# Performance work log

Measured on AMD Instinct MI355X. Metric: run time of the kernel, lower is better.

Reference implementation:

```python
import jax, jax.numpy as jnp
import numpy as np

D_MODEL = 1024
NUM_HEADS = 16
DK = D_MODEL // NUM_HEADS
B, S = 2, 2048


def _init_w(key, out_f, in_f):
    std = 2.0 / (in_f + out_f) ** 0.5
    w = jax.random.truncated_normal(key, -3.0, 3.0, (out_f, in_f), dtype=jnp.float32)
    return w * std


def setup_inputs() -> dict:
    key = jax.random.key(0)
    kx, kq, kk, kv, ko = jax.random.split(key, 5)
    return {
        "x": jax.random.normal(kx, (B, S, D_MODEL), dtype=jnp.float32),
        "Wq": _init_w(kq, D_MODEL, D_MODEL),
        "Wk": _init_w(kk, D_MODEL, D_MODEL),
        "Wv": _init_w(kv, D_MODEL, D_MODEL),
        "Wo": _init_w(ko, D_MODEL, D_MODEL),
    }


def reference(x, Wq, Wk, Wv, Wo):
    b, s, _ = x.shape
    # Linear: einsum('... d_in, d_out d_in -> ... d_out')
    q = jnp.einsum("bsd,ed->bse", x, Wq)
    k = jnp.einsum("bsd,ed->bse", x, Wk)
    v = jnp.einsum("bsd,ed->bse", x, Wv)
    # split heads: [b, s, h*dk] -> [b, h, s, dk]
    q = q.reshape(b, s, NUM_HEADS, DK).transpose(0, 2, 1, 3)
    k = k.reshape(b, s, NUM_HEADS, DK).transpose(0, 2, 1, 3)
    v = v.reshape(b, s, NUM_HEADS, DK).transpose(0, 2, 1, 3)
    scores = jnp.einsum("bhqd,bhkd->bhqk", q, k) / (DK ** 0.5)
    causal = jnp.tril(jnp.ones((s, s), dtype=bool))
    scores = jnp.where(causal, scores, -jnp.inf)
    wei = jax.nn.softmax(scores, axis=-1)
    attn = jnp.einsum("bhqk,bhkd->bhqd", wei, v)
    attn = attn.transpose(0, 2, 1, 3).reshape(b, s, NUM_HEADS * DK)
    return jnp.einsum("bsd,ed->bse", attn, Wo)
```

## Files before the change

kernel.cpp:

```cpp
#include <hip/hip_runtime.h>
#include <hip/hip_bf16.h>
#include <math.h>

typedef __bf16 bf16;
typedef __attribute__((ext_vector_type(8))) __bf16 bf16x8;
typedef __attribute__((ext_vector_type(4))) __bf16 bf16x4;
typedef __attribute__((ext_vector_type(4))) float f32x4;

#define NHEAD 16
#define DKH 64
#define SEQ 2048
#define DMODEL 1024

__device__ __forceinline__ void gl_lds16(const void* g, void* lds) {
  __builtin_amdgcn_global_load_lds(
      (const __attribute__((address_space(1))) unsigned int*)g,
      (__attribute__((address_space(3))) unsigned int*)lds, 16, 0, 0);
}

__global__ void cvt5_kernel(const float* __restrict__ x, const float* __restrict__ wq,
                            const float* __restrict__ wk, const float* __restrict__ wv,
                            const float* __restrict__ wo, bf16* __restrict__ xb,
                            bf16* __restrict__ wqb, bf16* __restrict__ wkb,
                            bf16* __restrict__ wvb, bf16* __restrict__ wob) {
  int i = blockIdx.x * blockDim.x + threadIdx.x;
  const float* src; bf16* dst; int li;
  if (i < 1048576)      { src = x;  dst = xb;  li = i; }
  else if (i < 1310720) { src = wq; dst = wqb; li = i - 1048576; }
  else if (i < 1572864) { src = wk; dst = wkb; li = i - 1310720; }
  else if (i < 1835008) { src = wv; dst = wvb; li = i - 1572864; }
  else                  { src = wo; dst = wob; li = i - 1835008; }
  float4 v = ((const float4*)src)[li];
  bf16x4 o = { (bf16)v.x, (bf16)v.y, (bf16)v.z, (bf16)v.w };
  ((bf16x4*)dst)[li] = o;
}

__device__ __forceinline__ bf16x8 lds_frag(const bf16* T, int row, int gran) {
  return *(const bf16x8*)&T[row * 64 + ((gran ^ (row & 7)) << 3)];
}

template<int MODE>
__global__ __launch_bounds__(256) void gemm_nt(const bf16* __restrict__ A,
                                               const bf16* __restrict__ Bw,
                                               float* __restrict__ Cf,
                                               bf16* __restrict__ Cq,
                                               bf16* __restrict__ Ck,
                                               bf16* __restrict__ Cv,
                                               int M, int N, int K) {
  __shared__ __attribute__((aligned(16))) bf16 As[128 * 64];
  __shared__ __attribute__((aligned(16))) bf16 Bs[128 * 64];
  const int t = threadIdx.x;
  const int w = t >> 6, l = t & 63;
  const int wr = w >> 1, wc = w & 1;
  const int lin = blockIdx.y * gridDim.x + blockIdx.x;
  const int cpx = (gridDim.x * gridDim.y) >> 3;
  const int swz = (lin & 7) * cpx + (lin >> 3);
  const int tm = (swz / gridDim.x) * 128, tn = (swz % gridDim.x) * 128;
  const int c16 = l & 15, g4 = l >> 4, r8 = l >> 3;
  const int sg = ((l & 7) ^ (r8 & 7)) * 8;

  f32x4 acc[4][4];
#pragma unroll
  for (int i = 0; i < 4; ++i)
#pragma unroll
    for (int j = 0; j < 4; ++j) acc[i][j] = f32x4{0.f, 0.f, 0.f, 0.f};

  for (int k0 = 0; k0 < K; k0 += 64) {
#pragma unroll
    for (int c = 0; c < 4; ++c) {
      const int r0 = w * 32 + c * 8;
      gl_lds16(A + (size_t)(tm + r0 + r8) * K + k0 + sg, &As[r0 * 64]);
      gl_lds16(Bw + (size_t)(tn + r0 + r8) * K + k0 + sg, &Bs[r0 * 64]);
    }
    __syncthreads();
#pragma unroll
    for (int h = 0; h < 2; ++h) {
      bf16x8 af[4], bfr[4];
#pragma unroll
      for (int i = 0; i < 4; ++i)
        af[i] = lds_frag(As, wr * 64 + i * 16 + c16, h * 4 + g4);
#pragma unroll
      for (int j = 0; j < 4; ++j)
        bfr[j] = lds_frag(Bs, wc * 64 + j * 16 + c16, h * 4 + g4);
#pragma unroll
      for (int i = 0; i < 4; ++i)
#pragma unroll
        for (int j = 0; j < 4; ++j)
          acc[i][j] = __builtin_amdgcn_mfma_f32_16x16x32_bf16(af[i], bfr[j], acc[i][j], 0, 0, 0);
    }
    __syncthreads();
  }

  const int which = tn >> 10;
#pragma unroll
  for (int i = 0; i < 4; ++i) {
    const int row0 = tm + wr * 64 + i * 16 + g4 * 4;
#pragma unroll
    for (int j = 0; j < 4; ++j) {
      const int col = tn + wc * 64 + j * 16 + c16;
      if (MODE == 0) {
#pragma unroll
        for (int r = 0; r < 4; ++r) Cf[(size_t)(row0 + r) * N + col] = acc[i][j][r];
      } else {
        const int lc = col & 1023;
        if (which == 2) {
          const int bb = row0 >> 11, s = row0 & 2047;
          const int hh = lc >> 6, dk = lc & 63;
          bf16x4 o = { (bf16)acc[i][j][0], (bf16)acc[i][j][1],
                       (bf16)acc[i][j][2], (bf16)acc[i][j][3] };
          *(bf16x4*)&Cv[((size_t)(bb * NHEAD + hh) * DKH + dk) * SEQ + s] = o;
        } else {
          bf16* dst = which ? Ck : Cq;
#pragma unroll
          for (int r = 0; r < 4; ++r)
            dst[(size_t)(row0 + r) * DMODEL + lc] = (bf16)acc[i][j][r];
        }
      }
    }
  }
}

__device__ __forceinline__ f32x4 vmax4(f32x4 a, f32x4 b) {
  return f32x4{ fmaxf(a[0], b[0]), fmaxf(a[1], b[1]),
                fmaxf(a[2], b[2]), fmaxf(a[3], b[3]) };
}

__global__ __launch_bounds__(256) void attn_kernel(const bf16* __restrict__ qb,
                                                   const bf16* __restrict__ kb,
                                                   const bf16* __restrict__ vT,
                                                   bf16* __restrict__ ob) {
  __shared__ __attribute__((aligned(16))) bf16 Kt[2][64 * 64];
  __shared__ __attribute__((aligned(16))) bf16 Vt[2][64 * 64];
  __shared__ __attribute__((aligned(16))) bf16 Pb[4][16 * 64];
  const int w = threadIdx.x >> 6, l = threadIdx.x & 63;
  const int lin = blockIdx.x;
  const int swz = (lin & 7) * 64 + (lin >> 3);
  const int pr = swz & 15, h = (swz >> 4) & 15, b = swz >> 8;
  const int qtA = 31 - pr, qtB = pr;
  const int c16 = l & 15, g4 = l >> 4, r8 = l >> 3;
  const int sg = ((l & 7) ^ (r8 & 7)) * 8;

  const float SC2 = 0.125f * 1.44269504089f;
  const float THR = 8.0f / SC2;

  const bf16 oneb = (bf16)1.0f;
  const bf16x8 ones = { oneb, oneb, oneb, oneb, oneb, oneb, oneb, oneb };

  const bf16* kbase = kb + (size_t)b * SEQ * DMODEL + h * DKH;
  const bf16* vbase = vT + (size_t)(b * NHEAD + h) * DKH * SEQ;

  bf16x8 qfA[2], qfB[2];
#pragma unroll
  for (int d = 0; d < 2; ++d) {
    qfA[d] = *(const bf16x8*)(qb + (size_t)(b * SEQ + qtA * 64 + w * 16 + c16) * DMODEL +
                              h * DKH + d * 32 + g4 * 8);
    qfB[d] = *(const bf16x8*)(qb + (size_t)(b * SEQ + qtB * 64 + w * 16 + c16) * DMODEL +
                              h * DKH + d * 32 + g4 * 8);
  }

  auto stage = [&](int buf, int t) {
    const int kt0 = t * 64;
#pragma unroll
    for (int c = 0; c < 2; ++c) {
      const int row = w * 16 + c * 8;
      gl_lds16(kbase + (size_t)(kt0 + row + r8) * DMODEL + sg, &Kt[buf][row * 64]);
      gl_lds16(vbase + (size_t)(row + r8) * SEQ + kt0 + sg, &Vt[buf][row * 64]);
    }
  };

  stage(0, 0);
  __syncthreads();

  float mm = -INFINITY;
  f32x4 lsum4 = f32x4{0.f, 0.f, 0.f, 0.f};
  f32x4 acc[4];
#pragma unroll
  for (int n = 0; n < 4; ++n) acc[n] = f32x4{0.f, 0.f, 0.f, 0.f};

  const int TA = qtA + 1, TT = TA + qtB + 1;
  const int ql = w * 16 + c16;

  for (int tt = 0; tt < TT; ++tt) {
    const int cur = tt & 1;
    if (tt + 1 < TT) stage(cur ^ 1, (tt + 1 < TA) ? tt + 1 : tt + 1 - TA);
    const bool pA = tt < TA;
    const int t_in = pA ? tt : tt - TA;
    const bool diag = (t_in == (pA ? qtA : qtB));
    const bf16x8 q0 = pA ? qfA[0] : qfB[0];
    const bf16x8 q1 = pA ? qfA[1] : qfB[1];

    f32x4 s[4];
    __builtin_amdgcn_s_setprio(1);
#pragma unroll
    for (int j = 0; j < 4; ++j) {
      bf16x8 kf0 = lds_frag(Kt[cur], j * 16 + c16, g4);
      bf16x8 kf1 = lds_frag(Kt[cur], j * 16 + c16, 4 + g4);
      f32x4 c = f32x4{0.f, 0.f, 0.f, 0.f};
      c = __builtin_amdgcn_mfma_f32_16x16x32_bf16(kf0, q0, c, 0, 0, 0);
      c = __builtin_amdgcn_mfma_f32_16x16x32_bf16(kf1, q1, c, 0, 0, 0);
      s[j] = c;
    }
    __builtin_amdgcn_s_setprio(0);
    if (diag) {
#pragma unroll
      for (int j = 0; j < 4; ++j)
#pragma unroll
        for (int r = 0; r < 4; ++r)
          if (j * 16 + g4 * 4 + r > ql) s[j][r] = -INFINITY;
    }
    f32x4 t01 = vmax4(s[0], s[1]);
    f32x4 t23 = vmax4(s[2], s[3]);
    f32x4 tv = vmax4(t01, t23);
    float v = fmaxf(fmaxf(tv[0], tv[1]), fmaxf(tv[2], tv[3]));
    v = fmaxf(v, __shfl_xor(v, 16));
    v = fmaxf(v, __shfl_xor(v, 32));
    if (!__all(v <= mm + THR)) {
      const float mn = fmaxf(mm, v);
      const float scl = __builtin_amdgcn_exp2f(SC2 * (mm - mn));
      float sc4[4];
#pragma unroll
      for (int r = 0; r < 4; ++r) sc4[r] = __shfl(scl, g4 * 4 + r);
#pragma unroll
      for (int n = 0; n < 4; ++n)
#pragma unroll
        for (int r = 0; r < 4; ++r) acc[n][r] *= sc4[r];
#pragma unroll
      for (int r = 0; r < 4; ++r) lsum4[r] *= sc4[r];
      mm = mn;
    }
    const float nb = SC2 * mm;
    bf16* P = &Pb[w][0];
#pragma unroll
    for (int j = 0; j < 4; ++j) {
      bf16x4 pk;
#pragma unroll
      for (int r = 0; r < 4; ++r)
        pk[r] = (bf16)__builtin_amdgcn_exp2f(fmaf(s[j][r], SC2, -nb));
      const int col = j * 16 + g4 * 4;
      *(bf16x4*)&P[c16 * 64 + (((col >> 3) ^ (c16 & 7)) << 3) + (col & 7)] = pk;
    }
    bf16x8 pa0 = lds_frag(P, c16, g4);
    bf16x8 pa1 = lds_frag(P, c16, 4 + g4);
    __builtin_amdgcn_s_setprio(1);
#pragma unroll
    for (int n = 0; n < 4; ++n) {
      bf16x8 vf0 = lds_frag(Vt[cur], n * 16 + c16, g4);
      bf16x8 vf1 = lds_frag(Vt[cur], n * 16 + c16, 4 + g4);
      acc[n] = __builtin_amdgcn_mfma_f32_16x16x32_bf16(pa0, vf0, acc[n], 0, 0, 0);
      acc[n] = __builtin_amdgcn_mfma_f32_16x16x32_bf16(pa1, vf1, acc[n], 0, 0, 0);
    }
    lsum4 = __builtin_amdgcn_mfma_f32_16x16x32_bf16(pa0, ones, lsum4, 0, 0, 0);
    lsum4 = __builtin_amdgcn_mfma_f32_16x16x32_bf16(pa1, ones, lsum4, 0, 0, 0);
    __builtin_amdgcn_s_setprio(0);

    if (tt == TA - 1) {
#pragma unroll
      for (int n = 0; n < 4; ++n)
#pragma unroll
        for (int r = 0; r < 4; ++r) {
          float o = acc[n][r] / lsum4[r];
          ob[(size_t)(b * SEQ + qtA * 64 + w * 16 + g4 * 4 + r) * DMODEL +
             h * DKH + n * 16 + c16] = (bf16)o;
          acc[n][r] = 0.f;
        }
      lsum4 = f32x4{0.f, 0.f, 0.f, 0.f};
      mm = -INFINITY;
    }
    __syncthreads();
  }

#pragma unroll
  for (int n = 0; n < 4; ++n)
#pragma unroll
    for (int r = 0; r < 4; ++r) {
      float o = acc[n][r] / lsum4[r];
      ob[(size_t)(b * SEQ + qtB * 64 + w * 16 + g4 * 4 + r) * DMODEL +
         h * DKH + n * 16 + c16] = (bf16)o;
    }
}

extern "C" void kernel_launch(void* const* d_in, const int* in_sizes, int n_in,
                              void* d_out, int out_size, void* d_ws, size_t ws_size,
                              hipStream_t stream) {
  const float* x  = (const float*)d_in[0];
  const float* Wq = (const float*)d_in[1];
  const float* Wk = (const float*)d_in[2];
  const float* Wv = (const float*)d_in[3];
  const float* Wo = (const float*)d_in[4];
  float* out = (float*)d_out;
  char* ws = (char*)d_ws;
  const size_t MB = (size_t)1 << 20;

  bf16* xb   = (bf16*)(ws + 0 * MB);
  bf16* wqb  = (bf16*)(ws + 8 * MB);
  bf16* wkb  = (bf16*)(ws + 10 * MB);
  bf16* wvb  = (bf16*)(ws + 12 * MB);
  bf16* wob  = (bf16*)(ws + 14 * MB);
  bf16* qbuf = (bf16*)(ws + 16 * MB);
  bf16* kbuf = (bf16*)(ws + 24 * MB);
  bf16* vTb  = (bf16*)(ws + 32 * MB);
  bf16* abuf = (bf16*)(ws + 40 * MB);

  cvt5_kernel<<<8192, 256, 0, stream>>>(x, Wq, Wk, Wv, Wo, xb, wqb, wkb, wvb, wob);

  gemm_nt<3><<<dim3(3072 / 128, 4096 / 128), 256, 0, stream>>>(
      xb, wqb, nullptr, qbuf, kbuf, vTb, 4096, 3072, 1024);

  attn_kernel<<<dim3(512), 256, 0, stream>>>(qbuf, kbuf, vTb, abuf);

  gemm_nt<0><<<dim3(1024 / 128, 4096 / 128), 256, 0, stream>>>(
      abuf, wob, out, nullptr, nullptr, nullptr, 4096, 1024, 1024);
}
```

Before: 181.8 us.

## Split attention KV tiles across two wave groups and double-buffer GEMM LDS

The attention kernel moves to 512 threads. Two groups of four waves each handle alternating 64-key tiles inside a 128-key step, and at the end of each query tile their partial softmax states (max, sum, accumulator) are merged through LDS. This doubles the waves working on each query tile, to hide latency and cut the serial KV loop length. Separately, the QKV/output GEMM gains double-buffered LDS staging, so the next K-slice loads while the current one is being multiplied. The costs are extra LDS use and merge synchronisation, wasted work for the odd group on diagonal tiles, and the partner accumulator rounded to bf16 during the merge.

Measured after the change: 181.4 us. Within noise of the previous version (-0.2%).

```diff
diff --git a/kernel.cpp b/kernel.cpp
--- a/kernel.cpp
+++ b/kernel.cpp
@@ -47,8 +47,8 @@
                                                bf16* __restrict__ Ck,
                                                bf16* __restrict__ Cv,
                                                int M, int N, int K) {
-  __shared__ __attribute__((aligned(16))) bf16 As[128 * 64];
-  __shared__ __attribute__((aligned(16))) bf16 Bs[128 * 64];
+  __shared__ __attribute__((aligned(16))) bf16 As[2][128 * 64];
+  __shared__ __attribute__((aligned(16))) bf16 Bs[2][128 * 64];
   const int t = threadIdx.x;
   const int w = t >> 6, l = t & 63;
   const int wr = w >> 1, wc = w & 1;
@@ -65,23 +65,31 @@
 #pragma unroll
     for (int j = 0; j < 4; ++j) acc[i][j] = f32x4{0.f, 0.f, 0.f, 0.f};
 
-  for (int k0 = 0; k0 < K; k0 += 64) {
+  auto stage = [&](int buf, int k0) {
 #pragma unroll
     for (int c = 0; c < 4; ++c) {
       const int r0 = w * 32 + c * 8;
-      gl_lds16(A + (size_t)(tm + r0 + r8) * K + k0 + sg, &As[r0 * 64]);
-      gl_lds16(Bw + (size_t)(tn + r0 + r8) * K + k0 + sg, &Bs[r0 * 64]);
-    }
-    __syncthreads();
-#pragma unroll
-    for (int h = 0; h < 2; ++h) {
+      gl_lds16(A + (size_t)(tm + r0 + r8) * K + k0 + sg, &As[buf][r0 * 64]);
+      gl_lds16(Bw + (size_t)(tn + r0 + r8) * K + k0 + sg, &Bs[buf][r0 * 64]);
+    }
+  };
+
+  const int NK = K >> 6;
+  stage(0, 0);
+  __syncthreads();
+
+  for (int kt = 0; kt < NK; ++kt) {
+    const int cur = kt & 1;
+    if (kt + 1 < NK) stage(cur ^ 1, (kt + 1) << 6);
+#pragma unroll
+    for (int hh = 0; hh < 2; ++hh) {
       bf16x8 af[4], bfr[4];
 #pragma unroll
       for (int i = 0; i < 4; ++i)
-        af[i] = lds_frag(As, wr * 64 + i * 16 + c16, h * 4 + g4);
+        af[i] = lds_frag(As[cur], wr * 64 + i * 16 + c16, hh * 4 + g4);
 #pragma unroll
       for (int j = 0; j < 4; ++j)
-        bfr[j] = lds_frag(Bs, wc * 64 + j * 16 + c16, h * 4 + g4);
+        bfr[j] = lds_frag(Bs[cur], wc * 64 + j * 16 + c16, hh * 4 + g4);
 #pragma unroll
       for (int i = 0; i < 4; ++i)
 #pragma unroll
@@ -125,14 +133,17 @@
                 fmaxf(a[2], b[2]), fmaxf(a[3], b[3]) };
 }
 
-__global__ __launch_bounds__(256) void attn_kernel(const bf16* __restrict__ qb,
-                                                   const bf16* __restrict__ kb,
-                                                   const bf16* __restrict__ vT,
-                                                   bf16* __restrict__ ob) {
-  __shared__ __attribute__((aligned(16))) bf16 Kt[2][64 * 64];
-  __shared__ __attribute__((aligned(16))) bf16 Vt[2][64 * 64];
-  __shared__ __attribute__((aligned(16))) bf16 Pb[4][16 * 64];
+__global__ __launch_bounds__(512, 4) void attn_kernel(const bf16* __restrict__ qb,
+                                                      const bf16* __restrict__ kb,
+                                                      const bf16* __restrict__ vT,
+                                                      bf16* __restrict__ ob) {
+  __shared__ __attribute__((aligned(16))) bf16 Ke[2][64 * 64];
+  __shared__ __attribute__((aligned(16))) bf16 Ko[2][64 * 64];
+  __shared__ __attribute__((aligned(16))) bf16 Ve[2][64 * 64];
+  __shared__ __attribute__((aligned(16))) bf16 Vo[2][64 * 64];
+  __shared__ __attribute__((aligned(16))) bf16 Pb[8][16 * 64];
   const int w = threadIdx.x >> 6, l = threadIdx.x & 63;
+  const int g = w >> 2, wq = w & 3;
   const int lin = blockIdx.x;
   const int swz = (lin & 7) * 64 + (lin >> 3);
   const int pr = swz & 15, h = (swz >> 4) & 15, b = swz >> 8;
@@ -152,20 +163,19 @@
   bf16x8 qfA[2], qfB[2];
 #pragma unroll
   for (int d = 0; d < 2; ++d) {
-    qfA[d] = *(const bf16x8*)(qb + (size_t)(b * SEQ + qtA * 64 + w * 16 + c16) * DMODEL +
+    qfA[d] = *(const bf16x8*)(qb + (size_t)(b * SEQ + qtA * 64 + wq * 16 + c16) * DMODEL +
                               h * DKH + d * 32 + g4 * 8);
-    qfB[d] = *(const bf16x8*)(qb + (size_t)(b * SEQ + qtB * 64 + w * 16 + c16) * DMODEL +
+    qfB[d] = *(const bf16x8*)(qb + (size_t)(b * SEQ + qtB * 64 + wq * 16 + c16) * DMODEL +
                               h * DKH + d * 32 + g4 * 8);
   }
 
-  auto stage = [&](int buf, int t) {
-    const int kt0 = t * 64;
-#pragma unroll
-    for (int c = 0; c < 2; ++c) {
-      const int row = w * 16 + c * 8;
-      gl_lds16(kbase + (size_t)(kt0 + row + r8) * DMODEL + sg, &Kt[buf][row * 64]);
-      gl_lds16(vbase + (size_t)(row + r8) * SEQ + kt0 + sg, &Vt[buf][row * 64]);
-    }
+  auto stage = [&](int buf, int t128) {
+    const int kt0 = t128 * 128;
+    const int row = w * 8;
+    gl_lds16(kbase + (size_t)(kt0 + row + r8) * DMODEL + sg, &Ke[buf][row * 64]);
+    gl_lds16(kbase + (size_t)(kt0 + 64 + row + r8) * DMODEL + sg, &Ko[buf][row * 64]);
+    gl_lds16(vbase + (size_t)(row + r8) * SEQ + kt0 + sg, &Ve[buf][row * 64]);
+    gl_lds16(vbase + (size_t)(row + r8) * SEQ + kt0 + 64 + sg, &Vo[buf][row * 64]);
   };
 
   stage(0, 0);
@@ -177,106 +187,137 @@
 #pragma unroll
   for (int n = 0; n < 4; ++n) acc[n] = f32x4{0.f, 0.f, 0.f, 0.f};
 
-  const int TA = qtA + 1, TT = TA + qtB + 1;
-  const int ql = w * 16 + c16;
-
-  for (int tt = 0; tt < TT; ++tt) {
+  const int TA128 = (qtA + 2) >> 1;
+  const int TT128 = TA128 + ((qtB + 2) >> 1);
+  const int ql = wq * 16 + c16;
+
+  for (int tt = 0; tt < TT128; ++tt) {
     const int cur = tt & 1;
-    if (tt + 1 < TT) stage(cur ^ 1, (tt + 1 < TA) ? tt + 1 : tt + 1 - TA);
-    const bool pA = tt < TA;
-    const int t_in = pA ? tt : tt - TA;
-    const bool diag = (t_in == (pA ? qtA : qtB));
-    const bf16x8 q0 = pA ? qfA[0] : qfB[0];
-    const bf16x8 q1 = pA ? qfA[1] : qfB[1];
-
-    f32x4 s[4];
-    __builtin_amdgcn_s_setprio(1);
-#pragma unroll
-    for (int j = 0; j < 4; ++j) {
-      bf16x8 kf0 = lds_frag(Kt[cur], j * 16 + c16, g4);
-      bf16x8 kf1 = lds_frag(Kt[cur], j * 16 + c16, 4 + g4);
-      f32x4 c = f32x4{0.f, 0.f, 0.f, 0.f};
-      c = __builtin_amdgcn_mfma_f32_16x16x32_bf16(kf0, q0, c, 0, 0, 0);
-      c = __builtin_amdgcn_mfma_f32_16x16x32_bf16(kf1, q1, c, 0, 0, 0);
-      s[j] = c;
-    }
-    __builtin_amdgcn_s_setprio(0);
-    if (diag) {
-#pragma unroll
-      for (int j = 0; j < 4; ++j)
+    if (tt + 1 < TT128)
+      stage(cur ^ 1, (tt + 1 < TA128) ? tt + 1 : tt + 1 - TA128);
+    const bool pA = tt < TA128;
+    const int t_in = pA ? tt : tt - TA128;
+    const int qt = pA ? qtA : qtB;
+    const int kt64 = 2 * t_in + g;
+
+    if (kt64 <= qt) {
+      const bf16* Kl = g ? &Ko[cur][0] : &Ke[cur][0];
+      const bf16* Vl = g ? &Vo[cur][0] : &Ve[cur][0];
+      const bf16x8 q0 = pA ? qfA[0] : qfB[0];
+      const bf16x8 q1 = pA ? qfA[1] : qfB[1];
+
+      f32x4 s[4];
+      __builtin_amdgcn_s_setprio(1);
+#pragma unroll
+      for (int j = 0; j < 4; ++j) {
+        bf16x8 kf0 = lds_frag(Kl, j * 16 + c16, g4);
+        bf16x8 kf1 = lds_frag(Kl, j * 16 + c16, 4 + g4);
+        f32x4 c = f32x4{0.f, 0.f, 0.f, 0.f};
+        c = __builtin_amdgcn_mfma_f32_16x16x32_bf16(kf0, q0, c, 0, 0, 0);
+        c = __builtin_amdgcn_mfma_f32_16x16x32_bf16(kf1, q1, c, 0, 0, 0);
+        s[j] = c;
+      }
+      __builtin_amdgcn_s_setprio(0);
+      if (kt64 == qt) {
+#pragma unroll
+        for (int j = 0; j < 4; ++j)
+#pragma unroll
+          for (int r = 0; r < 4; ++r)
+            if (j * 16 + g4 * 4 + r > ql) s[j][r] = -INFINITY;
+      }
+      f32x4 t01 = vmax4(s[0], s[1]);
+      f32x4 t23 = vmax4(s[2], s[3]);
+      f32x4 tv = vmax4(t01, t23);
+      float v = fmaxf(fmaxf(tv[0], tv[1]), fmaxf(tv[2], tv[3]));
+      v = fmaxf(v, __shfl_xor(v, 16));
+      v = fmaxf(v, __shfl_xor(v, 32));
+      if (!__all(v <= mm + THR)) {
+        const float mn = fmaxf(mm, v);
+        const float scl = __builtin_amdgcn_exp2f(SC2 * (mm - mn));
+        float sc4[4];
+#pragma unroll
+        for (int r = 0; r < 4; ++r) sc4[r] = __shfl(scl, g4 * 4 + r);
+#pragma unroll
+        for (int n = 0; n < 4; ++n)
+#pragma unroll
+          for (int r = 0; r < 4; ++r) acc[n][r] *= sc4[r];
+#pragma unroll
+        for (int r = 0; r < 4; ++r) lsum4[r] *= sc4[r];
+        mm = mn;
+      }
+      const float nb = SC2 * mm;
+      bf16* P = &Pb[w][0];
+#pragma unroll
+      for (int j = 0; j < 4; ++j) {
+        bf16x4 pk;
 #pragma unroll
         for (int r = 0; r < 4; ++r)
-          if (j * 16 + g4 * 4 + r > ql) s[j][r] = -INFINITY;
-    }
-    f32x4 t01 = vmax4(s[0], s[1]);
-    f32x4 t23 = vmax4(s[2], s[3]);
-    f32x4 tv = vmax4(t01, t23);
-    float v = fmaxf(fmaxf(tv[0], tv[1]), fmaxf(tv[2], tv[3]));
-    v = fmaxf(v, __shfl_xor(v, 16));
-    v = fmaxf(v, __shfl_xor(v, 32));
-    if (!__all(v <= mm + THR)) {
-      const float mn = fmaxf(mm, v);
-      const float scl = __builtin_amdgcn_exp2f(SC2 * (mm - mn));
-      float sc4[4];
-#pragma unroll
-      for (int r = 0; r < 4; ++r) sc4[r] = __shfl(scl, g4 * 4 + r);
-#pragma unroll
-      for (int n = 0; n < 4; ++n)
-#pragma unroll
-        for (int r = 0; r < 4; ++r) acc[n][r] *= sc4[r];
-#pragma unroll
-      for (int r = 0; r < 4; ++r) lsum4[r] *= sc4[r];
-      mm = mn;
-    }
-    const float nb = SC2 * mm;
-    bf16* P = &Pb[w][0];
-#pragma unroll
-    for (int j = 0; j < 4; ++j) {
-      bf16x4 pk;
-#pragma unroll
-      for (int r = 0; r < 4; ++r)
-        pk[r] = (bf16)__builtin_amdgcn_exp2f(fmaf(s[j][r], SC2, -nb));
-      const int col = j * 16 + g4 * 4;
-      *(bf16x4*)&P[c16 * 64 + (((col >> 3) ^ (c16 & 7)) << 3) + (col & 7)] = pk;
-    }
-    bf16x8 pa0 = lds_frag(P, c16, g4);
-    bf16x8 pa1 = lds_frag(P, c16, 4 + g4);
-    __builtin_amdgcn_s_setprio(1);
-#pragma unroll
-    for (int n = 0; n < 4; ++n) {
-      bf16x8 vf0 = lds_frag(Vt[cur], n * 16 + c16, g4);
-      bf16x8 vf1 = lds_frag(Vt[cur], n * 16 + c16, 4 + g4);
-      acc[n] = __builtin_amdgcn_mfma_f32_16x16x32_bf16(pa0, vf0, acc[n], 0, 0, 0);
-      acc[n] = __builtin_amdgcn_mfma_f32_16x16x32_bf16(pa1, vf1, acc[n], 0, 0, 0);
-    }
-    lsum4 = __builtin_amdgcn_mfma_f32_16x16x32_bf16(pa0, ones, lsum4, 0, 0, 0);
-    lsum4 = __builtin_amdgcn_mfma_f32_16x16x32_bf16(pa1, ones, lsum4, 0, 0, 0);
-    __builtin_amdgcn_s_setprio(0);
-
-    if (tt == TA - 1) {
-#pragma unroll
-      for (int n = 0; n < 4; ++n)
+          pk[r] = (bf16)__builtin_amdgcn_exp2f(fmaf(s[j][r], SC2, -nb));
+        const int col = j * 16 + g4 * 4;
+        *(bf16x4*)&P[c16 * 64 + (((col >> 3) ^ (c16 & 7)) << 3) + (col & 7)] = pk;
+      }
+      bf16x8 pa0 = lds_frag(P, c16, g4);
+      bf16x8 pa1 = lds_frag(P, c16, 4 + g4);
+      __builtin_amdgcn_s_setprio(1);
+#pragma unroll
+      for (int n = 0; n < 4; ++n) {
+        bf16x8 vf0 = lds_frag(Vl, n * 16 + c16, g4);
+        bf16x8 vf1 = lds_frag(Vl, n * 16 + c16, 4 + g4);
+        acc[n] = __builtin_amdgcn_mfma_f32_16x16x32_bf16(pa0, vf0, acc[n], 0, 0, 0);
+        acc[n] = __builtin_amdgcn_mfma_f32_16x16x32_bf16(pa1, vf1, acc[n], 0, 0, 0);
+      }
+      lsum4 = __builtin_amdgcn_mfma_f32_16x16x32_bf16(pa0, ones, lsum4, 0, 0, 0);
+      lsum4 = __builtin_amdgcn_mfma_f32_16x16x32_bf16(pa1, ones, lsum4, 0, 0, 0);
+      __builtin_amdgcn_s_setprio(0);
+    }
+
+    const bool mergeA = (tt == TA128 - 1);
+    const bool mergeB = (tt == TT128 - 1);
+    if (mergeA || mergeB) {
+      const int qb0 = (mergeA ? qtA : qtB) * 64;
+      __syncthreads();
+      float* ml = (float*)&Pb[wq][0];
+      bf16* xa = &Pb[4 + wq][0];
+      if (g == 1) {
+        if (g4 == 0) ml[c16] = mm;
+        if (c16 == 0) {
+#pragma unroll
+          for (int r = 0; r < 4; ++r) ml[16 + g4 * 4 + r] = lsum4[r];
+        }
+#pragma unroll
+        for (int n = 0; n < 4; ++n)
+#pragma unroll
+          for (int r = 0; r < 4; ++r)
+            xa[(g4 * 4 + r) * 64 + n * 16 + c16] = (bf16)acc[n][r];
+      }
+      __syncthreads();
+      if (g == 0) {
 #pragma unroll
         for (int r = 0; r < 4; ++r) {
-          float o = acc[n][r] / lsum4[r];
-          ob[(size_t)(b * SEQ + qtA * 64 + w * 16 + g4 * 4 + r) * DMODEL +
-             h * DKH + n * 16 + c16] = (bf16)o;
-          acc[n][r] = 0.f;
+          const int q = g4 * 4 + r;
+          const float mA = __shfl(mm, q);
+          const float mB = ml[q];
+          const float lB = ml[16 + q];
+          const float mt = fmaxf(mA, mB);
+          const float fA = __builtin_amdgcn_exp2f(SC2 * (mA - mt));
+          const float fB = __builtin_amdgcn_exp2f(SC2 * (mB - mt));
+          const float inv = 1.f / (lsum4[r] * fA + lB * fB);
+#pragma unroll
+          for (int n = 0; n < 4; ++n) {
+            const float accB = (float)xa[q * 64 + n * 16 + c16];
+            const float o = (acc[n][r] * fA + accB * fB) * inv;
+            ob[(size_t)(b * SEQ + qb0 + wq * 16 + q) * DMODEL +
+               h * DKH + n * 16 + c16] = (bf16)o;
+          }
         }
+      }
+      mm = -INFINITY;
       lsum4 = f32x4{0.f, 0.f, 0.f, 0.f};
-      mm = -INFINITY;
+#pragma unroll
+      for (int n = 0; n < 4; ++n) acc[n] = f32x4{0.f, 0.f, 0.f, 0.f};
     }
     __syncthreads();
   }
-
-#pragma unroll
-  for (int n = 0; n < 4; ++n)
-#pragma unroll
-    for (int r = 0; r < 4; ++r) {
-      float o = acc[n][r] / lsum4[r];
-      ob[(size_t)(b * SEQ + qtB * 64 + w * 16 + g4 * 4 + r) * DMODEL +
-         h * DKH + n * 16 + c16] = (bf16)o;
-    }
 }
 
 extern "C" void kernel_launch(void* const* d_in, const int* in_sizes, int n_in,
@@ -306,7 +347,7 @@
   gemm_nt<3><<<dim3(3072 / 128, 4096 / 128), 256, 0, stream>>>(
       xb, wqb, nullptr, qbuf, kbuf, vTb, 4096, 3072, 1024);
 
-  attn_kernel<<<dim3(512), 256, 0, stream>>>(qbuf, kbuf, vTb, abuf);
+  attn_kernel<<<dim3(512), 512, 0, stream>>>(qbuf, kbuf, vTb, abuf);
 
   gemm_nt<0><<<dim3(1024 / 128, 4096 / 128), 256, 0, stream>>>(
       abuf, wob, out, nullptr, nullptr, nullptr, 4096, 1024, 1024);
```
